# Kernel tuning notes

Measured on AMD Instinct MI355X. Metric: run time of the kernel, lower is better.

## Reference

```python
import jax, jax.numpy as jnp
import numpy as np

REF_MIC = 0
LOAD = 0.001 / np.sqrt(2.0)  # diagonal loading added to both real and imag parts


def _to_complex(x):
    # x: (N, 2, ...) real/imag stacked -> complex (N, ...)
    return x[:, 0] + 1j * x[:, 1]


def setup_inputs() -> dict:
    key = jax.random.key(0)
    k1, k2, k3 = jax.random.split(key, 3)
    N, C, T, F = 8, 16, 300, 257
    mixture = jax.random.normal(k1, (N, 2, C, T, F), dtype=jnp.float32)
    target = jax.random.normal(k2, (N, 2, C, T, F), dtype=jnp.float32)
    steering_vector = jax.random.normal(k3, (N, 2, C, F), dtype=jnp.float32)
    return {"mixture": mixture, "target": target, "steering_vector": steering_vector}


def reference(mixture, target, steering_vector):
    N, _, C, T, F = mixture.shape
    y = _to_complex(mixture)  # (N, C, T, F)
    x = _to_complex(target)   # (N, C, T, F)

    # Spatial covariance of mixture, mean over time frames (sum/T), fused einsum
    # phi[n,f] = (1/T) * sum_t y[n,:,t,f] y[n,:,t,f]^H  -> (N, F, C, C)
    phi = jnp.einsum('nctf,ndtf->nfcd', y, jnp.conj(y)) / T
    eye = jnp.eye(C, dtype=phi.dtype)
    # original adds load to BOTH real and imag diagonals (broadcast over RI dim)
    phi = phi + (LOAD + 1j * LOAD) * eye
    phi_inv = jnp.linalg.inv(phi)  # (N, F, C, C)

    # Cross covariance between mixture and reference-mic target
    A = jnp.transpose(y, (0, 3, 2, 1))            # (N, F, T, C)
    b = jnp.transpose(x[:, REF_MIC], (0, 2, 1))   # (N, F, T)
    mu_a = jnp.mean(A, axis=(0, 2), keepdims=True)  # mean over batch and time
    mu_b = jnp.mean(b, axis=(0, 2), keepdims=True)
    # mean over T of (A-mu_a)(b-mu_b)^H -> (N, F, C)
    phi_yx0 = jnp.mean((A - mu_a) * jnp.conj(b - mu_b)[..., None], axis=2)

    # MWF weights: w = phi_inv @ phi_yx0  -> (N, F, C)
    w = jnp.einsum('nfcd,nfd->nfc', phi_inv, phi_yx0)

    # Beamform: X_bf[n,t,f] = w[n,f]^H y[n,:,t,f]
    Xbf = jnp.einsum('nfc,nctf->ntf', jnp.conj(w), y)  # (N, T, F)

    # Back to real/imag stacked (N, 2, 1, T, F) matching torch output layout
    out = jnp.stack([Xbf.real, Xbf.imag], axis=1)[:, :, None]
    return out
```

## Files before the change

kernel.cpp:

```cpp
#include <hip/hip_runtime.h>

#define N_     8
#define C_     16
#define T_     300
#define F_     257
#define TF_    (T_*F_)
#define CTF_   (C_*TF_)
#define N2CTF_ (2*CTF_)

#define FT_    32
#define NFT_   9
#define TS_    5
#define RST_   35
#define SROWS_ 88
#define SCNT_  (SROWS_*RST_)
#define NTILE_ 10
#define PHIC_  (NTILE_*16)

#define MREC_  272

#define LOADC  7.0710678118654755e-04f

__device__ __forceinline__ float2 cmul(float2 a, float2 b) {
  return make_float2(a.x*b.x - a.y*b.y, a.x*b.y + a.y*b.x);
}
__device__ __forceinline__ float2 cmulc(float2 a, float2 b) {
  return make_float2(a.x*b.x + a.y*b.y, a.y*b.x - a.x*b.y);
}
__device__ __forceinline__ float2 cdiv(float2 a, float2 b) {
  float inv = 1.0f / (b.x*b.x + b.y*b.y);
  return make_float2((a.x*b.x + a.y*b.y)*inv, (a.y*b.x - a.x*b.y)*inv);
}
__device__ __forceinline__ float2 cadd(float2 a, float2 b){ return make_float2(a.x+b.x, a.y+b.y); }
__device__ __forceinline__ float2 csub(float2 a, float2 b){ return make_float2(a.x-b.x, a.y-b.y); }

template<int TCH>
__global__ __launch_bounds__(320, 1) void k1_cov(const float* __restrict__ mix,
                                                 const float* __restrict__ tgt,
                                                 float2* __restrict__ phi_p,
                                                 float2* __restrict__ syx_p,
                                                 float2* __restrict__ sy_p,
                                                 float2* __restrict__ sx_p) {
  __shared__ float2 ys[2][SCNT_];
  const int tid = threadIdx.x;
  const int ft = blockIdx.x, tc = blockIdx.y, n = blockIdx.z;
  const int fbase = ft * FT_;
  const int t0 = tc * TCH;
  const int fl = tid & 31;
  const int g  = tid >> 5;
  int ti = 0, tj = g;
  while (tj > ti) { ++ti; tj -= ti; }
  const int c0 = ti * 4;
  const int d0 = tj * 4;
  const bool sThread = (tj == 0);
  const bool xg = (g < 5);

  const float* mixN = mix + n * N2CTF_;
  const float* tgtN = tgt + n * N2CTF_;

  const int ts_g   = g >> 1;
  const int c_base = (g & 1) * 8;
  const int row0   = ts_g * 16 + c_base;
  const int f_ld = min(fbase + fl, F_ - 1);
  const float* ybase = mixN + c_base * TF_ + f_ld;
  const float* xbase = tgtN + f_ld;

  float2 acc[4][4];
  #pragma unroll
  for (int i = 0; i < 4; ++i)
    #pragma unroll
    for (int j = 0; j < 4; ++j) acc[i][j] = make_float2(0.f, 0.f);
  float2 syx[4], sy[4], sx = make_float2(0.f, 0.f);
  #pragma unroll
  for (int i = 0; i < 4; ++i) { syx[i] = make_float2(0.f,0.f); sy[i] = make_float2(0.f,0.f); }

  float lr[9], li[9];
  {
    #pragma unroll
    for (int k = 0; k < 8; ++k) {
      const float* p = ybase + k * TF_ + (t0 + ts_g) * F_;
      lr[k] = p[0]; li[k] = p[CTF_];
    }
    if (xg) { const float* p = xbase + (t0 + g) * F_; lr[8] = p[0]; li[8] = p[CTF_]; }
    #pragma unroll
    for (int k = 0; k < 8; ++k)
      ys[0][(row0 + k) * RST_ + fl] = make_float2(lr[k], li[k]);
    if (xg) ys[0][(80 + g) * RST_ + fl] = make_float2(lr[8], li[8]);
  }

  constexpr int NS = TCH / TS_;
  for (int stg = 0; stg < NS; ++stg) {
    __syncthreads();
    const bool more = (stg + 1 < NS);
    if (more) {
      const int tS = t0 + (stg + 1) * TS_;
      #pragma unroll
      for (int k = 0; k < 8; ++k) {
        const float* p = ybase + k * TF_ + (tS + ts_g) * F_;
        lr[k] = p[0]; li[k] = p[CTF_];
      }
      if (xg) { const float* p = xbase + (tS + g) * F_; lr[8] = p[0]; li[8] = p[CTF_]; }
    }
    const float2* buf = ys[stg & 1];
    #pragma unroll
    for (int tl = 0; tl < TS_; ++tl) {
      const int rb = tl * 16;
      float2 a[4], b[4];
      #pragma unroll
      for (int i = 0; i < 4; ++i) a[i] = buf[(rb + c0 + i) * RST_ + fl];
      #pragma unroll
      for (int j = 0; j < 4; ++j) b[j] = buf[(rb + d0 + j) * RST_ + fl];
      #pragma unroll
      for (int i = 0; i < 4; ++i)
        #pragma unroll
        for (int j = 0; j < 4; ++j) {
          acc[i][j].x += a[i].x * b[j].x + a[i].y * b[j].y;
          acc[i][j].y += a[i].y * b[j].x - a[i].x * b[j].y;
        }
      if (sThread) {
        float2 xv = buf[(80 + tl) * RST_ + fl];
        #pragma unroll
        for (int i = 0; i < 4; ++i) {
          syx[i].x += a[i].x * xv.x + a[i].y * xv.y;
          syx[i].y += a[i].y * xv.x - a[i].x * xv.y;
          sy[i].x += a[i].x; sy[i].y += a[i].y;
        }
        if (g == 0) { sx.x += xv.x; sx.y += xv.y; }
      }
    }
    if (more) {
      float2* nb = ys[(stg + 1) & 1];
      #pragma unroll
      for (int k = 0; k < 8; ++k)
        nb[(row0 + k) * RST_ + fl] = make_float2(lr[k], li[k]);
      if (xg) nb[(80 + g) * RST_ + fl] = make_float2(lr[8], li[8]);
    }
  }

  const int f = fbase + fl;
  if (f < F_) {
    const int tcn = tc * N_ + n;
    float2* pb = phi_p + ((size_t)tcn * F_ + f) * PHIC_ + g * 16;
    #pragma unroll
    for (int i = 0; i < 4; ++i)
      #pragma unroll
      for (int j = 0; j < 4; ++j) pb[i * 4 + j] = acc[i][j];
    if (sThread) {
      float2* s1 = syx_p + ((size_t)tcn * F_ + f) * C_ + c0;
      float2* s2 = sy_p  + ((size_t)tcn * F_ + f) * C_ + c0;
      #pragma unroll
      for (int i = 0; i < 4; ++i) { s1[i] = syx[i]; s2[i] = sy[i]; }
      if (g == 0) sx_p[(size_t)tcn * F_ + f] = sx;
    }
  }
}

template<int TCP>
__global__ __launch_bounds__(256) void k2a_reduce(const float2* __restrict__ phi_p,
                                                  const float2* __restrict__ syx_p,
                                                  const float2* __restrict__ sy_p,
                                                  const float2* __restrict__ sx_p,
                                                  float2* __restrict__ Mg) {
  __shared__ float2 ld_sy[TCP * N_ * C_];
  __shared__ float2 ld_syx[TCP * C_];
  __shared__ float2 ld_sx[TCP * N_];
  __shared__ float2 muB_s, sxO_s;
  const int f = blockIdx.x, n = blockIdx.y;
  const int tid = threadIdx.x;
  const int i = tid >> 4, j = tid & 15;

  const int ti = i >> 2, tj = j >> 2, ci = i & 3, cj = j & 3;
  int gL, cell; bool cj_flip;
  if (ti >= tj) { gL = ti * (ti + 1) / 2 + tj; cell = ci * 4 + cj; cj_flip = false; }
  else          { gL = tj * (tj + 1) / 2 + ti; cell = cj * 4 + ci; cj_flip = true; }
  const int off = gL * 16 + cell;

  float2 s = make_float2(0.f, 0.f);
  for (int tc = 0; tc < TCP; ++tc) {
    float2 v = phi_p[((size_t)(tc * N_ + n) * F_ + f) * PHIC_ + off];
    s.x += v.x; s.y += v.y;
  }
  if (cj_flip) s.y = -s.y;
  if (i == j) { s.x += (float)T_ * LOADC; s.y += (float)T_ * LOADC; }

  for (int idx = tid; idx < TCP * N_ * C_; idx += 256) {
    int tcn = idx >> 4, c = idx & 15;
    ld_sy[idx] = sy_p[((size_t)tcn * F_ + f) * C_ + c];
  }
  for (int idx = tid; idx < TCP * C_; idx += 256) {
    int tc = idx >> 4, c = idx & 15;
    ld_syx[idx] = syx_p[((size_t)(tc * N_ + n) * F_ + f) * C_ + c];
  }
  for (int idx = tid; idx < TCP * N_; idx += 256) {
    ld_sx[idx] = sx_p[(size_t)idx * F_ + f];
  }
  __syncthreads();

  float2 muA_r = make_float2(0.f,0.f), ownY = make_float2(0.f,0.f), ownYX = make_float2(0.f,0.f);
  if (tid < 16) {
    float2 allY = make_float2(0.f,0.f);
    for (int tcn = 0; tcn < TCP * N_; ++tcn) allY = cadd(allY, ld_sy[tcn * C_ + tid]);
    for (int tc = 0; tc < TCP; ++tc) {
      ownY  = cadd(ownY,  ld_sy[(tc * N_ + n) * C_ + tid]);
      ownYX = cadd(ownYX, ld_syx[tc * C_ + tid]);
    }
    const float invNT = 1.0f / ((float)N_ * (float)T_);
    muA_r = make_float2(allY.x * invNT, allY.y * invNT);
  }
  if (tid == 16) {
    float2 own = make_float2(0.f,0.f), all = make_float2(0.f,0.f);
    for (int tc = 0; tc < TCP; ++tc)
      for (int nn = 0; nn < N_; ++nn) {
        float2 v = ld_sx[tc * N_ + nn];
        all = cadd(all, v);
        if (nn == n) own = cadd(own, v);
      }
    const float invNT = 1.0f / ((float)N_ * (float)T_);
    muB_s = make_float2(all.x * invNT, all.y * invNT);
    sxO_s = own;
  }
  __syncthreads();

  float2* dst = Mg + (size_t)(n * F_ + f) * MREC_;
  dst[tid] = s;
  if (tid < 16) {
    float2 r = ownYX;
    r = csub(r, cmulc(muA_r, sxO_s));
    r = csub(r, cmulc(ownY, muB_s));
    float2 t3 = cmulc(muA_r, muB_s);
    r.x += (float)T_ * t3.x; r.y += (float)T_ * t3.y;
    dst[256 + tid] = r;
  }
}

__global__ __launch_bounds__(64) void k2b_solve(const float2* __restrict__ Mg,
                                                float* __restrict__ wre,
                                                float* __restrict__ wim) {
  __shared__ float2 M[16 * 17];
  const int f = blockIdx.x, n = blockIdx.y;
  const int tid = threadIdx.x;
  const float2* src = Mg + (size_t)(n * F_ + f) * MREC_;
  #pragma unroll
  for (int r = 0; r < 4; ++r) {
    int idx = tid + 64 * r;
    M[(idx >> 4) * 17 + (idx & 15)] = src[idx];
  }
  if (tid < 16) M[tid * 17 + 16] = src[256 + tid];
  __syncthreads();

  const int i = tid >> 2, q = tid & 3;
  for (int k = 0; k < 16; ++k) {
    float2 fac = cdiv(M[i * 17 + k], M[k * 17 + k]);
    __syncthreads();
    if (i != k) {
      #pragma unroll
      for (int jj = 0; jj < 4; ++jj) {
        int j = q * 4 + jj;
        M[i * 17 + j] = csub(M[i * 17 + j], cmul(fac, M[k * 17 + j]));
      }
      if (q == 3) M[i * 17 + 16] = csub(M[i * 17 + 16], cmul(fac, M[k * 17 + 16]));
    }
    __syncthreads();
  }
  if (q == 0) {
    float2 w = cdiv(M[i * 17 + 16], M[i * 17 + i]);
    wre[(n * C_ + i) * F_ + f] = w.x;
    wim[(n * C_ + i) * F_ + f] = w.y;
  }
}

__global__ __launch_bounds__(256) void k3_bf(const float* __restrict__ mix,
                                             const float* __restrict__ wre,
                                             const float* __restrict__ wim,
                                             float* __restrict__ out) {
  const int t0 = blockIdx.x * 2, n = blockIdx.y;
  const float* mixN = mix + n * N2CTF_;
  const float* wR = wre + n * C_ * F_;
  const float* wI = wim + n * C_ * F_;
  float* outN = out + n * 2 * TF_;
  for (int f = threadIdx.x; f < F_; f += 256) {
    float wr[16], wi[16];
    #pragma unroll
    for (int c = 0; c < 16; ++c) { wr[c] = wR[c * F_ + f]; wi[c] = wI[c * F_ + f]; }
    const float* yb = mixN + t0 * F_ + f;
    float xr0 = 0.f, xi0 = 0.f, xr1 = 0.f, xi1 = 0.f;
    #pragma unroll
    for (int c = 0; c < 16; ++c) {
      float yr0 = yb[c * TF_],      yi0 = yb[CTF_ + c * TF_];
      float yr1 = yb[c * TF_ + F_], yi1 = yb[CTF_ + c * TF_ + F_];
      xr0 += wr[c] * yr0 + wi[c] * yi0;
      xi0 += wr[c] * yi0 - wi[c] * yr0;
      xr1 += wr[c] * yr1 + wi[c] * yi1;
      xi1 += wr[c] * yi1 - wi[c] * yr1;
    }
    outN[t0 * F_ + f] = xr0;
    outN[TF_ + t0 * F_ + f] = xi0;
    outN[(t0 + 1) * F_ + f] = xr1;
    outN[TF_ + (t0 + 1) * F_ + f] = xi1;
  }
}

template<int TCP>
static void launch_all(const float* mix, const float* tgt, float* ws, float* out,
                       hipStream_t stream) {
  constexpr int TCH = T_ / TCP;
  static_assert(TCH * TCP == T_ && TCH % TS_ == 0, "chunking");
  float2* phi_p = (float2*)ws;
  float2* syx_p = phi_p + (size_t)TCP * N_ * F_ * PHIC_;
  float2* sy_p  = syx_p + (size_t)TCP * N_ * F_ * C_;
  float2* sx_p  = sy_p  + (size_t)TCP * N_ * F_ * C_;
  float2* Mg    = sx_p  + (size_t)TCP * N_ * F_;
  float*  wre   = (float*)(Mg + (size_t)N_ * F_ * MREC_);
  float*  wim   = wre + N_ * C_ * F_;
  k1_cov<TCH><<<dim3(NFT_, TCP, N_), dim3(320), 0, stream>>>(mix, tgt, phi_p, syx_p, sy_p, sx_p);
  k2a_reduce<TCP><<<dim3(F_, N_), dim3(256), 0, stream>>>(phi_p, syx_p, sy_p, sx_p, Mg);
  k2b_solve<<<dim3(F_, N_), dim3(64), 0, stream>>>(Mg, wre, wim);
  k3_bf<<<dim3(T_ / 2, N_), dim3(256), 0, stream>>>(mix, wre, wim, out);
}

static size_t ws_need_bytes(int tcp) {
  size_t fl2 = (size_t)tcp * N_ * F_ * (PHIC_ + C_ + C_ + 1) + (size_t)N_ * F_ * MREC_;
  return fl2 * 8 + 2ull * N_ * C_ * F_ * 4;
}

extern "C" void kernel_launch(void* const* d_in, const int* in_sizes, int n_in,
                              void* d_out, int out_size, void* d_ws, size_t ws_size,
                              hipStream_t stream) {
  const float* mix = (const float*)d_in[0];
  const float* tgt = (const float*)d_in[1];
  float* out = (float*)d_out;
  float* ws  = (float*)d_ws;
  if (ws_size >= ws_need_bytes(10))      launch_all<10>(mix, tgt, ws, out, stream);
  else if (ws_size >= ws_need_bytes(5))  launch_all<5>(mix, tgt, ws, out, stream);
  else if (ws_size >= ws_need_bytes(2))  launch_all<2>(mix, tgt, ws, out, stream);
  else                                   launch_all<1>(mix, tgt, ws, out, stream);
}
```

Baseline: 240.0 us.

## Vectorize covariance FMAs, single-buffer LDS, one-pass beamformer, more time chunks

The covariance kernel now uses two-wide float vectors arranged so each complex multiply-accumulate can map to packed FMA instructions, which is meant to cut ALU instruction count. The double-buffered shared tile is replaced by a single buffer plus an extra barrier per stage, halving LDS use at the cost of less overlap between loads and compute. The beamformer runs one thread per frequency in 320-thread blocks instead of a strided loop, removing the second partial pass. The default time split rises from 10 to 12 chunks to increase the number of blocks, at the cost of more partial results to reduce.

Result: no change. 237.8 us (-0.9%).

```diff
diff --git a/kernel.cpp b/kernel.cpp
--- a/kernel.cpp
+++ b/kernel.cpp
@@ -21,6 +21,8 @@
 
 #define LOADC  7.0710678118654755e-04f
 
+typedef float v2f __attribute__((ext_vector_type(2)));
+
 __device__ __forceinline__ float2 cmul(float2 a, float2 b) {
   return make_float2(a.x*b.x - a.y*b.y, a.x*b.y + a.y*b.x);
 }
@@ -37,11 +39,15 @@
 template<int TCH>
 __global__ __launch_bounds__(320, 1) void k1_cov(const float* __restrict__ mix,
                                                  const float* __restrict__ tgt,
-                                                 float2* __restrict__ phi_p,
-                                                 float2* __restrict__ syx_p,
-                                                 float2* __restrict__ sy_p,
-                                                 float2* __restrict__ sx_p) {
-  __shared__ float2 ys[2][SCNT_];
+                                                 float2* __restrict__ phi_pf,
+                                                 float2* __restrict__ syx_pf,
+                                                 float2* __restrict__ sy_pf,
+                                                 float2* __restrict__ sx_pf) {
+  __shared__ v2f ys[SCNT_];
+  v2f* phi_p = (v2f*)phi_pf;
+  v2f* syx_p = (v2f*)syx_pf;
+  v2f* sy_p  = (v2f*)sy_pf;
+  v2f* sx_p  = (v2f*)sx_pf;
   const int tid = threadIdx.x;
   const int ft = blockIdx.x, tc = blockIdx.y, n = blockIdx.z;
   const int fbase = ft * FT_;
@@ -65,14 +71,14 @@
   const float* ybase = mixN + c_base * TF_ + f_ld;
   const float* xbase = tgtN + f_ld;
 
-  float2 acc[4][4];
+  v2f acc[4][4];
   #pragma unroll
   for (int i = 0; i < 4; ++i)
     #pragma unroll
-    for (int j = 0; j < 4; ++j) acc[i][j] = make_float2(0.f, 0.f);
-  float2 syx[4], sy[4], sx = make_float2(0.f, 0.f);
-  #pragma unroll
-  for (int i = 0; i < 4; ++i) { syx[i] = make_float2(0.f,0.f); sy[i] = make_float2(0.f,0.f); }
+    for (int j = 0; j < 4; ++j) acc[i][j] = (v2f){0.f, 0.f};
+  v2f syx[4], sy[4], sx = (v2f){0.f, 0.f};
+  #pragma unroll
+  for (int i = 0; i < 4; ++i) { syx[i] = (v2f){0.f,0.f}; sy[i] = (v2f){0.f,0.f}; }
 
   float lr[9], li[9];
   {
@@ -84,8 +90,8 @@
     if (xg) { const float* p = xbase + (t0 + g) * F_; lr[8] = p[0]; li[8] = p[CTF_]; }
     #pragma unroll
     for (int k = 0; k < 8; ++k)
-      ys[0][(row0 + k) * RST_ + fl] = make_float2(lr[k], li[k]);
-    if (xg) ys[0][(80 + g) * RST_ + fl] = make_float2(lr[8], li[8]);
+      ys[(row0 + k) * RST_ + fl] = (v2f){lr[k], li[k]};
+    if (xg) ys[(80 + g) * RST_ + fl] = (v2f){lr[8], li[8]};
   }
 
   constexpr int NS = TCH / TS_;
@@ -101,53 +107,55 @@
       }
       if (xg) { const float* p = xbase + (tS + g) * F_; lr[8] = p[0]; li[8] = p[CTF_]; }
     }
-    const float2* buf = ys[stg & 1];
     #pragma unroll
     for (int tl = 0; tl < TS_; ++tl) {
       const int rb = tl * 16;
-      float2 a[4], b[4];
-      #pragma unroll
-      for (int i = 0; i < 4; ++i) a[i] = buf[(rb + c0 + i) * RST_ + fl];
-      #pragma unroll
-      for (int j = 0; j < 4; ++j) b[j] = buf[(rb + d0 + j) * RST_ + fl];
+      v2f a[4], bu[4], bv[4];
+      #pragma unroll
+      for (int i = 0; i < 4; ++i) a[i] = ys[(rb + c0 + i) * RST_ + fl];
+      #pragma unroll
+      for (int j = 0; j < 4; ++j) {
+        v2f b = ys[(rb + d0 + j) * RST_ + fl];
+        bu[j] = (v2f){b.x, -b.y};
+        bv[j] = (v2f){b.y,  b.x};
+      }
       #pragma unroll
       for (int i = 0; i < 4; ++i)
         #pragma unroll
-        for (int j = 0; j < 4; ++j) {
-          acc[i][j].x += a[i].x * b[j].x + a[i].y * b[j].y;
-          acc[i][j].y += a[i].y * b[j].x - a[i].x * b[j].y;
-        }
+        for (int j = 0; j < 4; ++j)
+          acc[i][j] += a[i].x * bu[j] + a[i].y * bv[j];
       if (sThread) {
-        float2 xv = buf[(80 + tl) * RST_ + fl];
+        v2f xv = ys[(80 + tl) * RST_ + fl];
+        v2f xu = (v2f){xv.x, -xv.y};
+        v2f xw = (v2f){xv.y,  xv.x};
         #pragma unroll
         for (int i = 0; i < 4; ++i) {
-          syx[i].x += a[i].x * xv.x + a[i].y * xv.y;
-          syx[i].y += a[i].y * xv.x - a[i].x * xv.y;
-          sy[i].x += a[i].x; sy[i].y += a[i].y;
+          syx[i] += a[i].x * xu + a[i].y * xw;
+          sy[i]  += a[i];
         }
-        if (g == 0) { sx.x += xv.x; sx.y += xv.y; }
-      }
-    }
+        if (g == 0) sx += xv;
+      }
+    }
+    __syncthreads();
     if (more) {
-      float2* nb = ys[(stg + 1) & 1];
       #pragma unroll
       for (int k = 0; k < 8; ++k)
-        nb[(row0 + k) * RST_ + fl] = make_float2(lr[k], li[k]);
-      if (xg) nb[(80 + g) * RST_ + fl] = make_float2(lr[8], li[8]);
+        ys[(row0 + k) * RST_ + fl] = (v2f){lr[k], li[k]};
+      if (xg) ys[(80 + g) * RST_ + fl] = (v2f){lr[8], li[8]};
     }
   }
 
   const int f = fbase + fl;
   if (f < F_) {
     const int tcn = tc * N_ + n;
-    float2* pb = phi_p + ((size_t)tcn * F_ + f) * PHIC_ + g * 16;
+    v2f* pb = phi_p + ((size_t)tcn * F_ + f) * PHIC_ + g * 16;
     #pragma unroll
     for (int i = 0; i < 4; ++i)
       #pragma unroll
       for (int j = 0; j < 4; ++j) pb[i * 4 + j] = acc[i][j];
     if (sThread) {
-      float2* s1 = syx_p + ((size_t)tcn * F_ + f) * C_ + c0;
-      float2* s2 = sy_p  + ((size_t)tcn * F_ + f) * C_ + c0;
+      v2f* s1 = syx_p + ((size_t)tcn * F_ + f) * C_ + c0;
+      v2f* s2 = sy_p  + ((size_t)tcn * F_ + f) * C_ + c0;
       #pragma unroll
       for (int i = 0; i < 4; ++i) { s1[i] = syx[i]; s2[i] = sy[i]; }
       if (g == 0) sx_p[(size_t)tcn * F_ + f] = sx;
@@ -269,35 +277,35 @@
   }
 }
 
-__global__ __launch_bounds__(256) void k3_bf(const float* __restrict__ mix,
+__global__ __launch_bounds__(320) void k3_bf(const float* __restrict__ mix,
                                              const float* __restrict__ wre,
                                              const float* __restrict__ wim,
                                              float* __restrict__ out) {
   const int t0 = blockIdx.x * 2, n = blockIdx.y;
+  const int f = threadIdx.x;
+  if (f >= F_) return;
   const float* mixN = mix + n * N2CTF_;
   const float* wR = wre + n * C_ * F_;
   const float* wI = wim + n * C_ * F_;
   float* outN = out + n * 2 * TF_;
-  for (int f = threadIdx.x; f < F_; f += 256) {
-    float wr[16], wi[16];
-    #pragma unroll
-    for (int c = 0; c < 16; ++c) { wr[c] = wR[c * F_ + f]; wi[c] = wI[c * F_ + f]; }
-    const float* yb = mixN + t0 * F_ + f;
-    float xr0 = 0.f, xi0 = 0.f, xr1 = 0.f, xi1 = 0.f;
-    #pragma unroll
-    for (int c = 0; c < 16; ++c) {
-      float yr0 = yb[c * TF_],      yi0 = yb[CTF_ + c * TF_];
-      float yr1 = yb[c * TF_ + F_], yi1 = yb[CTF_ + c * TF_ + F_];
-      xr0 += wr[c] * yr0 + wi[c] * yi0;
-      xi0 += wr[c] * yi0 - wi[c] * yr0;
-      xr1 += wr[c] * yr1 + wi[c] * yi1;
-      xi1 += wr[c] * yi1 - wi[c] * yr1;
-    }
-    outN[t0 * F_ + f] = xr0;
-    outN[TF_ + t0 * F_ + f] = xi0;
-    outN[(t0 + 1) * F_ + f] = xr1;
-    outN[TF_ + (t0 + 1) * F_ + f] = xi1;
-  }
+  float wr[16], wi[16];
+  #pragma unroll
+  for (int c = 0; c < 16; ++c) { wr[c] = wR[c * F_ + f]; wi[c] = wI[c * F_ + f]; }
+  const float* yb = mixN + t0 * F_ + f;
+  float xr0 = 0.f, xi0 = 0.f, xr1 = 0.f, xi1 = 0.f;
+  #pragma unroll
+  for (int c = 0; c < 16; ++c) {
+    float yr0 = yb[c * TF_],      yi0 = yb[CTF_ + c * TF_];
+    float yr1 = yb[c * TF_ + F_], yi1 = yb[CTF_ + c * TF_ + F_];
+    xr0 += wr[c] * yr0 + wi[c] * yi0;
+    xi0 += wr[c] * yi0 - wi[c] * yr0;
+    xr1 += wr[c] * yr1 + wi[c] * yi1;
+    xi1 += wr[c] * yi1 - wi[c] * yr1;
+  }
+  outN[t0 * F_ + f] = xr0;
+  outN[TF_ + t0 * F_ + f] = xi0;
+  outN[(t0 + 1) * F_ + f] = xr1;
+  outN[TF_ + (t0 + 1) * F_ + f] = xi1;
 }
 
 template<int TCP>
@@ -315,7 +323,7 @@
   k1_cov<TCH><<<dim3(NFT_, TCP, N_), dim3(320), 0, stream>>>(mix, tgt, phi_p, syx_p, sy_p, sx_p);
   k2a_reduce<TCP><<<dim3(F_, N_), dim3(256), 0, stream>>>(phi_p, syx_p, sy_p, sx_p, Mg);
   k2b_solve<<<dim3(F_, N_), dim3(64), 0, stream>>>(Mg, wre, wim);
-  k3_bf<<<dim3(T_ / 2, N_), dim3(256), 0, stream>>>(mix, wre, wim, out);
+  k3_bf<<<dim3(T_ / 2, N_), dim3(320), 0, stream>>>(mix, wre, wim, out);
 }
 
 static size_t ws_need_bytes(int tcp) {
@@ -330,8 +338,9 @@
   const float* tgt = (const float*)d_in[1];
   float* out = (float*)d_out;
   float* ws  = (float*)d_ws;
-  if (ws_size >= ws_need_bytes(10))      launch_all<10>(mix, tgt, ws, out, stream);
-  else if (ws_size >= ws_need_bytes(5))  launch_all<5>(mix, tgt, ws, out, stream);
+  if (ws_size >= ws_need_bytes(12))      launch_all<12>(mix, tgt, ws, out, stream);
+  else if (ws_size >= ws_need_bytes(10)) launch_all<10>(mix, tgt, ws, out, stream);
+  else if (ws_size >= ws_need_bytes(6))  launch_all<6>(mix, tgt, ws, out, stream);
   else if (ws_size >= ws_need_bytes(2))  launch_all<2>(mix, tgt, ws, out, stream);
   else                                   launch_all<1>(mix, tgt, ws, out, stream);
 }
```
